# Performance work log

Measured on AMD Instinct MI355X. Metric: run time of the kernel, lower is better.

Reference implementation:

```python
import jax, jax.numpy as jnp
import numpy as np

N_NODES = 89250


def _sage_conv(x, src, dst, w_l, w_r, b):
    # mean aggregation of neighbor messages x[src] at destination nodes
    msg = x[src]                                                # [E, C]
    agg = jax.ops.segment_sum(msg, dst, num_segments=N_NODES)   # [N, C]
    cnt = jax.ops.segment_sum(jnp.ones((src.shape[0],), x.dtype), dst,
                              num_segments=N_NODES)             # [N]
    mean = agg / jnp.clip(cnt, 1.0, None)[:, None]
    # PyG SAGEConv: lin_l(aggregated) + lin_r(x) + bias
    return mean @ w_l.T + x @ w_r.T + b


def setup_inputs() -> dict:
    key = jax.random.key(0)
    ks = jax.random.split(key, 9)
    N, E, F_IN = N_NODES, 899756, 500

    def glorot(k, shape):
        fan_in = shape[1]
        return jax.random.normal(k, shape, jnp.float32) / jnp.sqrt(jnp.float32(fan_in))

    x = jax.random.normal(ks[0], (N, F_IN), jnp.float32)
    edge_index = jax.random.randint(ks[1], (2, E), 0, N, jnp.int64 if jax.config.jax_enable_x64 else jnp.int32)
    return {
        "x": x,
        "edge_index": edge_index,
        "w_l1": glorot(ks[2], (512, F_IN)),
        "w_r1": glorot(ks[3], (512, F_IN)),
        "b1": jnp.zeros((512,), jnp.float32),
        "w_l2": glorot(ks[4], (256, 512)),
        "w_r2": glorot(ks[5], (256, 512)),
        "b2": jnp.zeros((256,), jnp.float32),
        "w_l3": glorot(ks[6], (7, 256)),
        "w_r3": glorot(ks[7], (7, 256)),
        "b3": jnp.zeros((7,), jnp.float32),
    }


def reference(x, edge_index, w_l1, w_r1, b1, w_l2, w_r2, b2, w_l3, w_r3, b3):
    src, dst = edge_index[0], edge_index[1]
    # eval mode: dropout is identity
    h = jax.nn.relu(_sage_conv(x, src, dst, w_l1, w_r1, b1))
    h = jax.nn.relu(_sage_conv(h, src, dst, w_l2, w_r2, b2))
    return _sage_conv(h, src, dst, w_l3, w_r3, b3)
```

## Files before the change

kernel.cpp:

```cpp
#include <hip/hip_runtime.h>
#include <cstdint>
#include <cstddef>

#define N_NODES 89250
#define M_PAD   89344
#define F0 500
#define F1 512
#define F2 256
#define F3 7
#define KP 512

typedef __attribute__((ext_vector_type(8))) short bf16x8;
typedef __attribute__((ext_vector_type(4))) float f32x4;

static inline int cdiv_i(int a, int b) { return (a + b - 1) / b; }

__device__ __forceinline__ unsigned short f2b(float f) {
  unsigned int u = __float_as_uint(f);
  u = (u + 0x7FFFu + ((u >> 16) & 1u)) >> 16;
  return (unsigned short)u;
}
__device__ __forceinline__ float b2f(unsigned short h) {
  return __uint_as_float(((unsigned int)h) << 16);
}

__global__ void degree_kernel(const int* __restrict__ dst, int* __restrict__ cnt, int E) {
  int stride = gridDim.x * blockDim.x;
  for (int i = blockIdx.x * blockDim.x + threadIdx.x; i < E; i += stride)
    atomicAdd(&cnt[dst[i]], 1);
}

__global__ __launch_bounds__(1024) void scan_partial(const int* __restrict__ cnt,
                                                     int* __restrict__ row_ptr,
                                                     int* __restrict__ bsum, int n) {
  __shared__ int sm[1024];
  const int i = blockIdx.x * 1024 + threadIdx.x;
  const int v = (i < n) ? cnt[i] : 0;
  sm[threadIdx.x] = v;
  __syncthreads();
  for (int off = 1; off < 1024; off <<= 1) {
    int t = (threadIdx.x >= off) ? sm[threadIdx.x - off] : 0;
    __syncthreads();
    sm[threadIdx.x] += t;
    __syncthreads();
  }
  if (i < n) row_ptr[i] = sm[threadIdx.x] - v;
  if (threadIdx.x == 1023) bsum[blockIdx.x] = sm[1023];
}

__global__ __launch_bounds__(1024) void scan_bsums(int* __restrict__ bsum, int nb) {
  __shared__ int sm[1024];
  const int v = (threadIdx.x < nb) ? bsum[threadIdx.x] : 0;
  sm[threadIdx.x] = v;
  __syncthreads();
  for (int off = 1; off < 1024; off <<= 1) {
    int t = (threadIdx.x >= off) ? sm[threadIdx.x - off] : 0;
    __syncthreads();
    sm[threadIdx.x] += t;
    __syncthreads();
  }
  if (threadIdx.x < nb) bsum[threadIdx.x] = sm[threadIdx.x] - v;
}

__global__ __launch_bounds__(1024) void scan_add(int* __restrict__ row_ptr,
                                                 const int* __restrict__ bsum,
                                                 int n, int total) {
  const int i = blockIdx.x * 1024 + threadIdx.x;
  if (i < n) row_ptr[i] += bsum[i >> 10];
  if (i == 0) row_ptr[n] = total;
}

__global__ void cursor_init_kernel(const int* __restrict__ row_ptr, int* __restrict__ cursor, int n) {
  int i = blockIdx.x * blockDim.x + threadIdx.x;
  if (i < n) cursor[i] = row_ptr[i];
}

__global__ void fill_kernel(const int* __restrict__ src, const int* __restrict__ dst,
                            int* __restrict__ cursor, int* __restrict__ csr_src, int E) {
  int stride = gridDim.x * blockDim.x;
  for (int i = blockIdx.x * blockDim.x + threadIdx.x; i < E; i += stride) {
    const int p = atomicAdd(&cursor[dst[i]], 1);
    csr_src[p] = src[i];
  }
}

__global__ __launch_bounds__(256) void convert_x_kernel(const float* __restrict__ x,
                                                        unsigned short* __restrict__ xb) {
  const long long total = (long long)M_PAD * (KP / 8);
  const long long stride = (long long)gridDim.x * blockDim.x;
  for (long long idx = (long long)blockIdx.x * blockDim.x + threadIdx.x; idx < total; idx += stride) {
    const int node = (int)(idx >> 6);
    const int c8 = ((int)idx & 63) * 8;
    unsigned short r[8];
#pragma unroll
    for (int j = 0; j < 8; ++j) {
      const int c = c8 + j;
      float v = 0.0f;
      if (node < N_NODES && c < F0) v = x[(size_t)node * F0 + c];
      r[j] = f2b(v);
    }
    *reinterpret_cast<uint4*>(xb + (size_t)node * KP + c8) = *reinterpret_cast<const uint4*>(r);
  }
}

__global__ __launch_bounds__(256) void convert_w_kernel(const float* __restrict__ w,
                                                        unsigned short* __restrict__ wb,
                                                        int J, int K) {
  const int total = J * KP;
  const int stride = gridDim.x * blockDim.x;
  for (int idx = blockIdx.x * blockDim.x + threadIdx.x; idx < total; idx += stride) {
    const int j = idx >> 9;
    const int k = idx & (KP - 1);
    wb[idx] = (k < K) ? f2b(w[(size_t)j * K + k]) : (unsigned short)0;
  }
}

__global__ __launch_bounds__(256) void gather_mean_bf512(
    const unsigned short* __restrict__ xb, const int* __restrict__ row_ptr,
    const int* __restrict__ csr_src, unsigned short* __restrict__ aggb)
{
  const int node = blockIdx.x * 4 + (threadIdx.x >> 6);
  const int t = threadIdx.x & 63;
  if (node >= M_PAD) return;
  if (node >= N_NODES) {
    *reinterpret_cast<uint4*>(aggb + (size_t)node * 512 + t * 8) = make_uint4(0, 0, 0, 0);
    return;
  }
  const int beg = row_ptr[node];
  const int end = row_ptr[node + 1];
  float acc[8] = {0.f, 0.f, 0.f, 0.f, 0.f, 0.f, 0.f, 0.f};
  int j = beg;
  for (; j + 1 < end; j += 2) {
    const int s0 = csr_src[j];
    const int s1 = csr_src[j + 1];
    const uint4 v0 = *reinterpret_cast<const uint4*>(xb + (size_t)s0 * 512 + t * 8);
    const uint4 v1 = *reinterpret_cast<const uint4*>(xb + (size_t)s1 * 512 + t * 8);
    const unsigned int u0[4] = {v0.x, v0.y, v0.z, v0.w};
    const unsigned int u1[4] = {v1.x, v1.y, v1.z, v1.w};
#pragma unroll
    for (int q = 0; q < 4; ++q) {
      acc[2 * q]     += b2f((unsigned short)(u0[q] & 0xFFFF)) + b2f((unsigned short)(u1[q] & 0xFFFF));
      acc[2 * q + 1] += b2f((unsigned short)(u0[q] >> 16))    + b2f((unsigned short)(u1[q] >> 16));
    }
  }
  if (j < end) {
    const int s0 = csr_src[j];
    const uint4 v0 = *reinterpret_cast<const uint4*>(xb + (size_t)s0 * 512 + t * 8);
    const unsigned int u0[4] = {v0.x, v0.y, v0.z, v0.w};
#pragma unroll
    for (int q = 0; q < 4; ++q) {
      acc[2 * q]     += b2f((unsigned short)(u0[q] & 0xFFFF));
      acc[2 * q + 1] += b2f((unsigned short)(u0[q] >> 16));
    }
  }
  const int deg = end - beg;
  const float inv = 1.0f / (float)(deg > 1 ? deg : 1);
  unsigned short r[8];
#pragma unroll
  for (int q = 0; q < 8; ++q) r[q] = f2b(acc[q] * inv);
  *reinterpret_cast<uint4*>(aggb + (size_t)node * 512 + t * 8) = *reinterpret_cast<const uint4*>(r);
}

__global__ __launch_bounds__(256) void gemm_mfma(
    const unsigned short* __restrict__ A1, const unsigned short* __restrict__ A2,
    const unsigned short* __restrict__ B1, const unsigned short* __restrict__ B2,
    const float* __restrict__ bias, unsigned short* __restrict__ Cout,
    int J, int niter, int fuse, int relu)
{
  __shared__ __align__(16) unsigned short Alds[128 * 64];
  __shared__ __align__(16) unsigned short Blds[128 * 64];
  const int tid = threadIdx.x;
  const int lane = tid & 63;
  const int wid = tid >> 6;

  const int nwg = gridDim.x * gridDim.y;
  int wg = blockIdx.y * gridDim.x + blockIdx.x;
  const int cpx = nwg >> 3;
  wg = (wg & 7) * cpx + (wg >> 3);
  const int brow = (wg % gridDim.x) * 128;
  const int bcol = (wg / gridDim.x) * 128;

  const int wr = wid >> 1;
  const int wc = wid & 1;

  f32x4 acc[4][4];
#pragma unroll
  for (int m = 0; m < 4; ++m)
#pragma unroll
    for (int n = 0; n < 4; ++n) acc[m][n] = (f32x4){0.f, 0.f, 0.f, 0.f};

  const int srow = lane >> 3;
  const int gchunk = (lane & 7) ^ srow;
  const int fr = lane & 15;
  const int fk = lane >> 4;

  for (int it = 0; it < niter; ++it) {
    const unsigned short* __restrict__ A = (it < 8) ? A1 : A2;
    const unsigned short* __restrict__ B = (it < 8) ? B1 : B2;
    const int k0 = (it & 7) * 64;
    __syncthreads();
#pragma unroll
    for (int i = 0; i < 4; ++i) {
      const int r = i * 32 + wid * 8;
      __builtin_amdgcn_global_load_lds(
          (const __attribute__((address_space(1))) unsigned int*)(A + (size_t)(brow + r + srow) * KP + k0 + gchunk * 8),
          (__attribute__((address_space(3))) unsigned int*)(&Alds[r * 64]),
          16, 0, 0);
      __builtin_amdgcn_global_load_lds(
          (const __attribute__((address_space(1))) unsigned int*)(B + (size_t)(bcol + r + srow) * KP + k0 + gchunk * 8),
          (__attribute__((address_space(3))) unsigned int*)(&Blds[r * 64]),
          16, 0, 0);
    }
    __syncthreads();
#pragma unroll
    for (int ks = 0; ks < 2; ++ks) {
      bf16x8 a[4], b[4];
#pragma unroll
      for (int m = 0; m < 4; ++m) {
        const int row = wr * 64 + m * 16 + fr;
        a[m] = *reinterpret_cast<const bf16x8*>(&Alds[row * 64 + (((ks * 4 + fk) ^ (fr & 7)) * 8)]);
      }
#pragma unroll
      for (int n = 0; n < 4; ++n) {
        const int row = wc * 64 + n * 16 + fr;
        b[n] = *reinterpret_cast<const bf16x8*>(&Blds[row * 64 + (((ks * 4 + fk) ^ (fr & 7)) * 8)]);
      }
#pragma unroll
      for (int m = 0; m < 4; ++m)
#pragma unroll
        for (int n = 0; n < 4; ++n)
          acc[m][n] = __builtin_amdgcn_mfma_f32_16x16x32_bf16(a[m], b[n], acc[m][n], 0, 0, 0);
    }
  }

  const int crow0 = brow + wr * 64 + (lane >> 4) * 4;
  const int ccol0 = bcol + wc * 64 + (lane & 15);
#pragma unroll
  for (int n = 0; n < 4; ++n) {
    const int col = ccol0 + n * 16;
    const float bv = fuse ? bias[col] : 0.0f;
#pragma unroll
    for (int m = 0; m < 4; ++m) {
#pragma unroll
      for (int i = 0; i < 4; ++i) {
        const int row = crow0 + m * 16 + i;
        float v = acc[m][n][i] + bv;
        if (relu) v = fmaxf(v, 0.0f);
        Cout[(size_t)row * J + col] = f2b(v);
      }
    }
  }
}

__global__ __launch_bounds__(256) void combine2_kernel(
    const unsigned short* __restrict__ y, const int* __restrict__ row_ptr,
    const int* __restrict__ csr_src, const float* __restrict__ bias,
    unsigned short* __restrict__ h)
{
  const int node = blockIdx.x * 8 + (threadIdx.x >> 5);
  const int t = threadIdx.x & 31;
  if (node >= N_NODES) return;
  const int beg = row_ptr[node];
  const int end = row_ptr[node + 1];
  float acc[8] = {0.f, 0.f, 0.f, 0.f, 0.f, 0.f, 0.f, 0.f};
  int j = beg;
  for (; j + 1 < end; j += 2) {
    const int s0 = csr_src[j];
    const int s1 = csr_src[j + 1];
    const uint4 v0 = *reinterpret_cast<const uint4*>(y + (size_t)s0 * 512 + t * 8);
    const uint4 v1 = *reinterpret_cast<const uint4*>(y + (size_t)s1 * 512 + t * 8);
    const unsigned int u0[4] = {v0.x, v0.y, v0.z, v0.w};
    const unsigned int u1[4] = {v1.x, v1.y, v1.z, v1.w};
#pragma unroll
    for (int q = 0; q < 4; ++q) {
      acc[2 * q]     += b2f((unsigned short)(u0[q] & 0xFFFF)) + b2f((unsigned short)(u1[q] & 0xFFFF));
      acc[2 * q + 1] += b2f((unsigned short)(u0[q] >> 16))    + b2f((unsigned short)(u1[q] >> 16));
    }
  }
  if (j < end) {
    const int s0 = csr_src[j];
    const uint4 v0 = *reinterpret_cast<const uint4*>(y + (size_t)s0 * 512 + t * 8);
    const unsigned int u0[4] = {v0.x, v0.y, v0.z, v0.w};
#pragma unroll
    for (int q = 0; q < 4; ++q) {
      acc[2 * q]     += b2f((unsigned short)(u0[q] & 0xFFFF));
      acc[2 * q + 1] += b2f((unsigned short)(u0[q] >> 16));
    }
  }
  const int deg = end - beg;
  const float inv = 1.0f / (float)(deg > 1 ? deg : 1);
  const uint4 rv = *reinterpret_cast<const uint4*>(y + (size_t)node * 512 + 256 + t * 8);
  const unsigned int ru[4] = {rv.x, rv.y, rv.z, rv.w};
  unsigned short r[8];
#pragma unroll
  for (int q = 0; q < 4; ++q) {
    const float y0 = b2f((unsigned short)(ru[q] & 0xFFFF));
    const float y1 = b2f((unsigned short)(ru[q] >> 16));
    const float c0 = acc[2 * q] * inv + y0 + bias[t * 8 + 2 * q];
    const float c1 = acc[2 * q + 1] * inv + y1 + bias[t * 8 + 2 * q + 1];
    r[2 * q]     = f2b(fmaxf(c0, 0.0f));
    r[2 * q + 1] = f2b(fmaxf(c1, 0.0f));
  }
  *reinterpret_cast<uint4*>(h + (size_t)node * 256 + t * 8) = *reinterpret_cast<const uint4*>(r);
}

__global__ __launch_bounds__(256) void gemm3_node(
    const unsigned short* __restrict__ h2, const float* __restrict__ wl,
    const float* __restrict__ wr, unsigned short* __restrict__ y3, int N)
{
  const int node = (blockIdx.x * 256 + threadIdx.x) >> 6;
  const int lane = threadIdx.x & 63;
  if (node >= N) return;
  const uint2 hu = *reinterpret_cast<const uint2*>(h2 + (size_t)node * F2 + lane * 4);
  const float h0 = b2f((unsigned short)(hu.x & 0xFFFF)), h1 = b2f((unsigned short)(hu.x >> 16));
  const float h2v = b2f((unsigned short)(hu.y & 0xFFFF)), h3 = b2f((unsigned short)(hu.y >> 16));
#pragma unroll
  for (int j = 0; j < F3; ++j) {
    const float4 l4 = *reinterpret_cast<const float4*>(wl + j * F2 + lane * 4);
    const float4 r4 = *reinterpret_cast<const float4*>(wr + j * F2 + lane * 4);
    float tl = h0 * l4.x + h1 * l4.y + h2v * l4.z + h3 * l4.w;
    float tr = h0 * r4.x + h1 * r4.y + h2v * r4.z + h3 * r4.w;
#pragma unroll
    for (int m = 1; m < 64; m <<= 1) {
      tl += __shfl_xor(tl, m, 64);
      tr += __shfl_xor(tr, m, 64);
    }
    if (lane == 0) {
      y3[(size_t)node * 16 + j]     = f2b(tl);
      y3[(size_t)node * 16 + 8 + j] = f2b(tr);
    }
  }
}

__global__ __launch_bounds__(256) void combine3_kernel(
    const unsigned short* __restrict__ y3, const int* __restrict__ row_ptr,
    const int* __restrict__ csr_src, const float* __restrict__ b3,
    float* __restrict__ out, int N)
{
  const int node = blockIdx.x * 256 + threadIdx.x;
  if (node >= N) return;
  const int beg = row_ptr[node];
  const int end = row_ptr[node + 1];
  float acc[8] = {0.f, 0.f, 0.f, 0.f, 0.f, 0.f, 0.f, 0.f};
  for (int j = beg; j < end; ++j) {
    const int s = csr_src[j];
    const uint4 v = *reinterpret_cast<const uint4*>(y3 + (size_t)s * 16);
    const unsigned int u[4] = {v.x, v.y, v.z, v.w};
#pragma unroll
    for (int q = 0; q < 4; ++q) {
      acc[2 * q]     += b2f((unsigned short)(u[q] & 0xFFFF));
      acc[2 * q + 1] += b2f((unsigned short)(u[q] >> 16));
    }
  }
  const int deg = end - beg;
  const float inv = 1.0f / (float)(deg > 1 ? deg : 1);
  const uint4 rv = *reinterpret_cast<const uint4*>(y3 + (size_t)node * 16 + 8);
  const unsigned int ru[4] = {rv.x, rv.y, rv.z, rv.w};
  float yr[8];
#pragma unroll
  for (int q = 0; q < 4; ++q) {
    yr[2 * q]     = b2f((unsigned short)(ru[q] & 0xFFFF));
    yr[2 * q + 1] = b2f((unsigned short)(ru[q] >> 16));
  }
#pragma unroll
  for (int q = 0; q < F3; ++q)
    out[(size_t)node * F3 + q] = acc[q] * inv + yr[q] + b3[q];
}

extern "C" void kernel_launch(void* const* d_in, const int* in_sizes, int n_in,
                              void* d_out, int out_size, void* d_ws, size_t ws_size,
                              hipStream_t stream) {
  const float* x    = (const float*)d_in[0];
  const int*   ei   = (const int*)d_in[1];
  const float* w_l1 = (const float*)d_in[2];
  const float* w_r1 = (const float*)d_in[3];
  const float* b1   = (const float*)d_in[4];
  const float* w_l2 = (const float*)d_in[5];
  const float* w_r2 = (const float*)d_in[6];
  const float* b2   = (const float*)d_in[7];
  const float* w_l3 = (const float*)d_in[8];
  const float* w_r3 = (const float*)d_in[9];
  const float* b3   = (const float*)d_in[10];
  float* out = (float*)d_out;

  const int E = in_sizes[1] / 2;
  const int* src = ei;
  const int* dst = ei + E;

  char* p = (char*)d_ws;
  int* row_ptr = (int*)p;           p += (size_t)(N_NODES + 1) * 4;
  int* cnt     = (int*)p;           p += (size_t)N_NODES * 4;
  int* bsum    = (int*)p;           p += 1024 * 4;
  int* csr_src = (int*)p;           p += (size_t)E * 4;
  p = (char*)(((uintptr_t)p + 255) & ~(uintptr_t)255);
  unsigned short* xb   = (unsigned short*)p;  p += (size_t)M_PAD * KP * 2;
  unsigned short* aggb = (unsigned short*)p;  p += (size_t)M_PAD * KP * 2;
  unsigned short* h1b  = (unsigned short*)p;  p += (size_t)M_PAD * KP * 2;
  unsigned short* wl1b = (unsigned short*)p;  p += (size_t)F1 * KP * 2;
  unsigned short* wr1b = (unsigned short*)p;  p += (size_t)F1 * KP * 2;
  unsigned short* w2b  = (unsigned short*)p;  p += (size_t)F1 * KP * 2;

  unsigned short* y2  = xb;
  unsigned short* h2b = aggb;
  unsigned short* y3  = h1b;

  const int nb = cdiv_i(N_NODES, 1024);

  hipMemsetAsync(cnt, 0, (size_t)N_NODES * sizeof(int), stream);
  degree_kernel<<<cdiv_i(E, 256), 256, 0, stream>>>(dst, cnt, E);
  scan_partial<<<nb, 1024, 0, stream>>>(cnt, row_ptr, bsum, N_NODES);
  scan_bsums<<<1, 1024, 0, stream>>>(bsum, nb);
  scan_add<<<nb, 1024, 0, stream>>>(row_ptr, bsum, N_NODES, E);
  cursor_init_kernel<<<cdiv_i(N_NODES, 256), 256, 0, stream>>>(row_ptr, cnt, N_NODES);
  fill_kernel<<<cdiv_i(E, 256), 256, 0, stream>>>(src, dst, cnt, csr_src, E);

  convert_x_kernel<<<2048, 256, 0, stream>>>(x, xb);
  convert_w_kernel<<<512, 256, 0, stream>>>(w_l1, wl1b, F1, F0);
  convert_w_kernel<<<512, 256, 0, stream>>>(w_r1, wr1b, F1, F0);
  convert_w_kernel<<<256, 256, 0, stream>>>(w_l2, w2b, F2, F1);
  convert_w_kernel<<<256, 256, 0, stream>>>(w_r2, w2b + (size_t)F2 * KP, F2, F1);

  gather_mean_bf512<<<cdiv_i(M_PAD, 4), 256, 0, stream>>>(xb, row_ptr, csr_src, aggb);
  {
    dim3 g(M_PAD / 128, F1 / 128);
    gemm_mfma<<<g, 256, 0, stream>>>(aggb, xb, wl1b, wr1b, b1, h1b, F1, 16, 1, 1);
  }

  {
    dim3 g(M_PAD / 128, 512 / 128);
    gemm_mfma<<<g, 256, 0, stream>>>(h1b, h1b, w2b, w2b, (const float*)nullptr, y2, 512, 8, 0, 0);
  }
  combine2_kernel<<<cdiv_i(N_NODES, 8), 256, 0, stream>>>(y2, row_ptr, csr_src, b2, h2b);

  gemm3_node<<<cdiv_i(N_NODES * 64, 256), 256, 0, stream>>>(h2b, w_l3, w_r3, y3, N_NODES);
  combine3_kernel<<<cdiv_i(N_NODES, 256), 256, 0, stream>>>(y3, row_ptr, csr_src, b3, out, N_NODES);
}
```

Before: 707.3 us.

## Fuse cursor init into scan, unroll gathers by four, remap GEMM tiles

Folds the cursor initialisation into scan_add, which removes one kernel launch. Unrolls the neighbour-gather loops in gather_mean and combine2 from two to four edges, so more independent row loads are in flight. Switches the aggregate stores to nontemporal and changes the GEMM workgroup-to-tile mapping so that consecutive workgroups share row blocks. The four-way unroll changes the floating-point summation order slightly and raises register use.

Result: faster. 686.4 us (-3.0%).

```diff
diff --git a/kernel.cpp b/kernel.cpp
--- a/kernel.cpp
+++ b/kernel.cpp
@@ -12,6 +12,7 @@
 
 typedef __attribute__((ext_vector_type(8))) short bf16x8;
 typedef __attribute__((ext_vector_type(4))) float f32x4;
+typedef __attribute__((ext_vector_type(4))) unsigned int uintx4;
 
 static inline int cdiv_i(int a, int b) { return (a + b - 1) / b; }
 
@@ -64,15 +65,15 @@
 
 __global__ __launch_bounds__(1024) void scan_add(int* __restrict__ row_ptr,
                                                  const int* __restrict__ bsum,
+                                                 int* __restrict__ cursor,
                                                  int n, int total) {
   const int i = blockIdx.x * 1024 + threadIdx.x;
-  if (i < n) row_ptr[i] += bsum[i >> 10];
+  if (i < n) {
+    const int v = row_ptr[i] + bsum[i >> 10];
+    row_ptr[i] = v;
+    cursor[i] = v;
+  }
   if (i == 0) row_ptr[n] = total;
-}
-
-__global__ void cursor_init_kernel(const int* __restrict__ row_ptr, int* __restrict__ cursor, int n) {
-  int i = blockIdx.x * blockDim.x + threadIdx.x;
-  if (i < n) cursor[i] = row_ptr[i];
 }
 
 __global__ void fill_kernel(const int* __restrict__ src, const int* __restrict__ dst,
@@ -123,27 +124,36 @@
   const int t = threadIdx.x & 63;
   if (node >= M_PAD) return;
   if (node >= N_NODES) {
-    *reinterpret_cast<uint4*>(aggb + (size_t)node * 512 + t * 8) = make_uint4(0, 0, 0, 0);
+    uintx4 z = (uintx4){0u, 0u, 0u, 0u};
+    __builtin_nontemporal_store(z, (uintx4*)(aggb + (size_t)node * 512 + t * 8));
     return;
   }
   const int beg = row_ptr[node];
   const int end = row_ptr[node + 1];
   float acc[8] = {0.f, 0.f, 0.f, 0.f, 0.f, 0.f, 0.f, 0.f};
   int j = beg;
-  for (; j + 1 < end; j += 2) {
+  for (; j + 3 < end; j += 4) {
     const int s0 = csr_src[j];
     const int s1 = csr_src[j + 1];
+    const int s2 = csr_src[j + 2];
+    const int s3 = csr_src[j + 3];
     const uint4 v0 = *reinterpret_cast<const uint4*>(xb + (size_t)s0 * 512 + t * 8);
     const uint4 v1 = *reinterpret_cast<const uint4*>(xb + (size_t)s1 * 512 + t * 8);
+    const uint4 v2 = *reinterpret_cast<const uint4*>(xb + (size_t)s2 * 512 + t * 8);
+    const uint4 v3 = *reinterpret_cast<const uint4*>(xb + (size_t)s3 * 512 + t * 8);
     const unsigned int u0[4] = {v0.x, v0.y, v0.z, v0.w};
     const unsigned int u1[4] = {v1.x, v1.y, v1.z, v1.w};
+    const unsigned int u2[4] = {v2.x, v2.y, v2.z, v2.w};
+    const unsigned int u3[4] = {v3.x, v3.y, v3.z, v3.w};
 #pragma unroll
     for (int q = 0; q < 4; ++q) {
-      acc[2 * q]     += b2f((unsigned short)(u0[q] & 0xFFFF)) + b2f((unsigned short)(u1[q] & 0xFFFF));
-      acc[2 * q + 1] += b2f((unsigned short)(u0[q] >> 16))    + b2f((unsigned short)(u1[q] >> 16));
-    }
-  }
-  if (j < end) {
+      acc[2 * q]     += (b2f((unsigned short)(u0[q] & 0xFFFF)) + b2f((unsigned short)(u1[q] & 0xFFFF)))
+                      + (b2f((unsigned short)(u2[q] & 0xFFFF)) + b2f((unsigned short)(u3[q] & 0xFFFF)));
+      acc[2 * q + 1] += (b2f((unsigned short)(u0[q] >> 16)) + b2f((unsigned short)(u1[q] >> 16)))
+                      + (b2f((unsigned short)(u2[q] >> 16)) + b2f((unsigned short)(u3[q] >> 16)));
+    }
+  }
+  for (; j < end; ++j) {
     const int s0 = csr_src[j];
     const uint4 v0 = *reinterpret_cast<const uint4*>(xb + (size_t)s0 * 512 + t * 8);
     const unsigned int u0[4] = {v0.x, v0.y, v0.z, v0.w};
@@ -158,7 +168,8 @@
   unsigned short r[8];
 #pragma unroll
   for (int q = 0; q < 8; ++q) r[q] = f2b(acc[q] * inv);
-  *reinterpret_cast<uint4*>(aggb + (size_t)node * 512 + t * 8) = *reinterpret_cast<const uint4*>(r);
+  __builtin_nontemporal_store(*reinterpret_cast<const uintx4*>(r),
+                              (uintx4*)(aggb + (size_t)node * 512 + t * 8));
 }
 
 __global__ __launch_bounds__(256) void gemm_mfma(
@@ -177,8 +188,8 @@
   int wg = blockIdx.y * gridDim.x + blockIdx.x;
   const int cpx = nwg >> 3;
   wg = (wg & 7) * cpx + (wg >> 3);
-  const int brow = (wg % gridDim.x) * 128;
-  const int bcol = (wg / gridDim.x) * 128;
+  const int brow = (wg / gridDim.y) * 128;
+  const int bcol = (wg % gridDim.y) * 128;
 
   const int wr = wid >> 1;
   const int wc = wid & 1;
@@ -264,20 +275,28 @@
   const int end = row_ptr[node + 1];
   float acc[8] = {0.f, 0.f, 0.f, 0.f, 0.f, 0.f, 0.f, 0.f};
   int j = beg;
-  for (; j + 1 < end; j += 2) {
+  for (; j + 3 < end; j += 4) {
     const int s0 = csr_src[j];
     const int s1 = csr_src[j + 1];
+    const int s2 = csr_src[j + 2];
+    const int s3 = csr_src[j + 3];
     const uint4 v0 = *reinterpret_cast<const uint4*>(y + (size_t)s0 * 512 + t * 8);
     const uint4 v1 = *reinterpret_cast<const uint4*>(y + (size_t)s1 * 512 + t * 8);
+    const uint4 v2 = *reinterpret_cast<const uint4*>(y + (size_t)s2 * 512 + t * 8);
+    const uint4 v3 = *reinterpret_cast<const uint4*>(y + (size_t)s3 * 512 + t * 8);
     const unsigned int u0[4] = {v0.x, v0.y, v0.z, v0.w};
     const unsigned int u1[4] = {v1.x, v1.y, v1.z, v1.w};
+    const unsigned int u2[4] = {v2.x, v2.y, v2.z, v2.w};
+    const unsigned int u3[4] = {v3.x, v3.y, v3.z, v3.w};
 #pragma unroll
     for (int q = 0; q < 4; ++q) {
-      acc[2 * q]     += b2f((unsigned short)(u0[q] & 0xFFFF)) + b2f((unsigned short)(u1[q] & 0xFFFF));
-      acc[2 * q + 1] += b2f((unsigned short)(u0[q] >> 16))    + b2f((unsigned short)(u1[q] >> 16));
-    }
-  }
-  if (j < end) {
+      acc[2 * q]     += (b2f((unsigned short)(u0[q] & 0xFFFF)) + b2f((unsigned short)(u1[q] & 0xFFFF)))
+                      + (b2f((unsigned short)(u2[q] & 0xFFFF)) + b2f((unsigned short)(u3[q] & 0xFFFF)));
+      acc[2 * q + 1] += (b2f((unsigned short)(u0[q] >> 16)) + b2f((unsigned short)(u1[q] >> 16)))
+                      + (b2f((unsigned short)(u2[q] >> 16)) + b2f((unsigned short)(u3[q] >> 16)));
+    }
+  }
+  for (; j < end; ++j) {
     const int s0 = csr_src[j];
     const uint4 v0 = *reinterpret_cast<const uint4*>(y + (size_t)s0 * 512 + t * 8);
     const unsigned int u0[4] = {v0.x, v0.y, v0.z, v0.w};
@@ -410,8 +429,7 @@
   degree_kernel<<<cdiv_i(E, 256), 256, 0, stream>>>(dst, cnt, E);
   scan_partial<<<nb, 1024, 0, stream>>>(cnt, row_ptr, bsum, N_NODES);
   scan_bsums<<<1, 1024, 0, stream>>>(bsum, nb);
-  scan_add<<<nb, 1024, 0, stream>>>(row_ptr, bsum, N_NODES, E);
-  cursor_init_kernel<<<cdiv_i(N_NODES, 256), 256, 0, stream>>>(row_ptr, cnt, N_NODES);
+  scan_add<<<nb, 1024, 0, stream>>>(row_ptr, bsum, cnt, N_NODES, E);
   fill_kernel<<<cdiv_i(E, 256), 256, 0, stream>>>(src, dst, cnt, csr_src, E);
 
   convert_x_kernel<<<2048, 256, 0, stream>>>(x, xb);
```

## Unroll gathers by eight, use MFMA for layer 3, merge setup kernels

Applied to the files above, without the earlier changes.

Several changes at once. Cursor init is fused into scan_add, the four weight-convert launches become one kernel that also pre-converts layer-3 weights, and the gather loops in layer 1 and layer 2 issue eight neighbor loads at a time with masking to raise memory-level parallelism. Layer-3 projection now uses a 16x16x32 bf16 MFMA instead of shuffle reductions, combine3 spreads each node's edges across a wave, and the GEMM workgroup-to-tile mapping is swapped. The masked loads still fetch data for edges past the end of each neighbor list, and the wave-per-node combine3 adds shuffle reductions.

Result: faster. 634.0 us (-10.4%).

```diff
diff --git a/kernel.cpp b/kernel.cpp
--- a/kernel.cpp
+++ b/kernel.cpp
@@ -64,15 +64,15 @@
 
 __global__ __launch_bounds__(1024) void scan_add(int* __restrict__ row_ptr,
                                                  const int* __restrict__ bsum,
+                                                 int* __restrict__ cursor,
                                                  int n, int total) {
   const int i = blockIdx.x * 1024 + threadIdx.x;
-  if (i < n) row_ptr[i] += bsum[i >> 10];
+  if (i < n) {
+    const int v = row_ptr[i] + bsum[i >> 10];
+    row_ptr[i] = v;
+    cursor[i] = v;
+  }
   if (i == 0) row_ptr[n] = total;
-}
-
-__global__ void cursor_init_kernel(const int* __restrict__ row_ptr, int* __restrict__ cursor, int n) {
-  int i = blockIdx.x * blockDim.x + threadIdx.x;
-  if (i < n) cursor[i] = row_ptr[i];
 }
 
 __global__ void fill_kernel(const int* __restrict__ src, const int* __restrict__ dst,
@@ -103,15 +103,36 @@
   }
 }
 
-__global__ __launch_bounds__(256) void convert_w_kernel(const float* __restrict__ w,
-                                                        unsigned short* __restrict__ wb,
-                                                        int J, int K) {
-  const int total = J * KP;
-  const int stride = gridDim.x * blockDim.x;
-  for (int idx = blockIdx.x * blockDim.x + threadIdx.x; idx < total; idx += stride) {
-    const int j = idx >> 9;
-    const int k = idx & (KP - 1);
-    wb[idx] = (k < K) ? f2b(w[(size_t)j * K + k]) : (unsigned short)0;
+__global__ __launch_bounds__(256) void convert_w_all(
+    const float* __restrict__ wl1, const float* __restrict__ wr1,
+    const float* __restrict__ wl2, const float* __restrict__ wr2,
+    const float* __restrict__ wl3, const float* __restrict__ wr3,
+    unsigned short* __restrict__ wl1b, unsigned short* __restrict__ wr1b,
+    unsigned short* __restrict__ w2b, unsigned short* __restrict__ w3b)
+{
+  int idx = blockIdx.x * 256 + threadIdx.x;
+  const int S1 = F1 * KP;
+  if (idx < S1) {
+    const int j = idx >> 9, k = idx & 511;
+    const bool in = (k < F0);
+    wl1b[idx] = in ? f2b(wl1[(size_t)j * F0 + k]) : (unsigned short)0;
+    wr1b[idx] = in ? f2b(wr1[(size_t)j * F0 + k]) : (unsigned short)0;
+    return;
+  }
+  idx -= S1;
+  const int S2 = F2 * KP;
+  if (idx < S2) {
+    w2b[idx] = f2b(wl2[idx]);
+    w2b[S2 + idx] = f2b(wr2[idx]);
+    return;
+  }
+  idx -= S2;
+  if (idx < 16 * 256) {
+    const int j = idx >> 8, k = idx & 255;
+    float v = 0.0f;
+    if (j < 7) v = wl3[(size_t)j * F2 + k];
+    else if (j >= 8 && j < 15) v = wr3[(size_t)(j - 8) * F2 + k];
+    w3b[idx] = f2b(v);
   }
 }
 
@@ -129,28 +150,23 @@
   const int beg = row_ptr[node];
   const int end = row_ptr[node + 1];
   float acc[8] = {0.f, 0.f, 0.f, 0.f, 0.f, 0.f, 0.f, 0.f};
-  int j = beg;
-  for (; j + 1 < end; j += 2) {
-    const int s0 = csr_src[j];
-    const int s1 = csr_src[j + 1];
-    const uint4 v0 = *reinterpret_cast<const uint4*>(xb + (size_t)s0 * 512 + t * 8);
-    const uint4 v1 = *reinterpret_cast<const uint4*>(xb + (size_t)s1 * 512 + t * 8);
-    const unsigned int u0[4] = {v0.x, v0.y, v0.z, v0.w};
-    const unsigned int u1[4] = {v1.x, v1.y, v1.z, v1.w};
-#pragma unroll
-    for (int q = 0; q < 4; ++q) {
-      acc[2 * q]     += b2f((unsigned short)(u0[q] & 0xFFFF)) + b2f((unsigned short)(u1[q] & 0xFFFF));
-      acc[2 * q + 1] += b2f((unsigned short)(u0[q] >> 16))    + b2f((unsigned short)(u1[q] >> 16));
-    }
-  }
-  if (j < end) {
-    const int s0 = csr_src[j];
-    const uint4 v0 = *reinterpret_cast<const uint4*>(xb + (size_t)s0 * 512 + t * 8);
-    const unsigned int u0[4] = {v0.x, v0.y, v0.z, v0.w};
-#pragma unroll
-    for (int q = 0; q < 4; ++q) {
-      acc[2 * q]     += b2f((unsigned short)(u0[q] & 0xFFFF));
-      acc[2 * q + 1] += b2f((unsigned short)(u0[q] >> 16));
+  for (int j = beg; j < end; j += 8) {
+    uint4 v[8];
+    float m[8];
+#pragma unroll
+    for (int u = 0; u < 8; ++u) {
+      const int e = min(j + u, end - 1);
+      m[u] = (j + u < end) ? 1.0f : 0.0f;
+      v[u] = *reinterpret_cast<const uint4*>(xb + (size_t)csr_src[e] * 512 + t * 8);
+    }
+#pragma unroll
+    for (int u = 0; u < 8; ++u) {
+      const unsigned int w[4] = {v[u].x, v[u].y, v[u].z, v[u].w};
+#pragma unroll
+      for (int q = 0; q < 4; ++q) {
+        acc[2 * q]     = fmaf(m[u], b2f((unsigned short)(w[q] & 0xFFFF)), acc[2 * q]);
+        acc[2 * q + 1] = fmaf(m[u], b2f((unsigned short)(w[q] >> 16)),    acc[2 * q + 1]);
+      }
     }
   }
   const int deg = end - beg;
@@ -177,8 +193,8 @@
   int wg = blockIdx.y * gridDim.x + blockIdx.x;
   const int cpx = nwg >> 3;
   wg = (wg & 7) * cpx + (wg >> 3);
-  const int brow = (wg % gridDim.x) * 128;
-  const int bcol = (wg / gridDim.x) * 128;
+  const int brow = (wg / gridDim.y) * 128;
+  const int bcol = (wg % gridDim.y) * 128;
 
   const int wr = wid >> 1;
   const int wc = wid & 1;
@@ -263,28 +279,23 @@
   const int beg = row_ptr[node];
   const int end = row_ptr[node + 1];
   float acc[8] = {0.f, 0.f, 0.f, 0.f, 0.f, 0.f, 0.f, 0.f};
-  int j = beg;
-  for (; j + 1 < end; j += 2) {
-    const int s0 = csr_src[j];
-    const int s1 = csr_src[j + 1];
-    const uint4 v0 = *reinterpret_cast<const uint4*>(y + (size_t)s0 * 512 + t * 8);
-    const uint4 v1 = *reinterpret_cast<const uint4*>(y + (size_t)s1 * 512 + t * 8);
-    const unsigned int u0[4] = {v0.x, v0.y, v0.z, v0.w};
-    const unsigned int u1[4] = {v1.x, v1.y, v1.z, v1.w};
-#pragma unroll
-    for (int q = 0; q < 4; ++q) {
-      acc[2 * q]     += b2f((unsigned short)(u0[q] & 0xFFFF)) + b2f((unsigned short)(u1[q] & 0xFFFF));
-      acc[2 * q + 1] += b2f((unsigned short)(u0[q] >> 16))    + b2f((unsigned short)(u1[q] >> 16));
-    }
-  }
-  if (j < end) {
-    const int s0 = csr_src[j];
-    const uint4 v0 = *reinterpret_cast<const uint4*>(y + (size_t)s0 * 512 + t * 8);
-    const unsigned int u0[4] = {v0.x, v0.y, v0.z, v0.w};
-#pragma unroll
-    for (int q = 0; q < 4; ++q) {
-      acc[2 * q]     += b2f((unsigned short)(u0[q] & 0xFFFF));
-      acc[2 * q + 1] += b2f((unsigned short)(u0[q] >> 16));
+  for (int j = beg; j < end; j += 8) {
+    uint4 v[8];
+    float m[8];
+#pragma unroll
+    for (int u = 0; u < 8; ++u) {
+      const int e = min(j + u, end - 1);
+      m[u] = (j + u < end) ? 1.0f : 0.0f;
+      v[u] = *reinterpret_cast<const uint4*>(y + (size_t)csr_src[e] * 512 + t * 8);
+    }
+#pragma unroll
+    for (int u = 0; u < 8; ++u) {
+      const unsigned int w[4] = {v[u].x, v[u].y, v[u].z, v[u].w};
+#pragma unroll
+      for (int q = 0; q < 4; ++q) {
+        acc[2 * q]     = fmaf(m[u], b2f((unsigned short)(w[q] & 0xFFFF)), acc[2 * q]);
+        acc[2 * q + 1] = fmaf(m[u], b2f((unsigned short)(w[q] >> 16)),    acc[2 * q + 1]);
+      }
     }
   }
   const int deg = end - beg;
@@ -304,32 +315,27 @@
   *reinterpret_cast<uint4*>(h + (size_t)node * 256 + t * 8) = *reinterpret_cast<const uint4*>(r);
 }
 
-__global__ __launch_bounds__(256) void gemm3_node(
-    const unsigned short* __restrict__ h2, const float* __restrict__ wl,
-    const float* __restrict__ wr, unsigned short* __restrict__ y3, int N)
-{
-  const int node = (blockIdx.x * 256 + threadIdx.x) >> 6;
-  const int lane = threadIdx.x & 63;
-  if (node >= N) return;
-  const uint2 hu = *reinterpret_cast<const uint2*>(h2 + (size_t)node * F2 + lane * 4);
-  const float h0 = b2f((unsigned short)(hu.x & 0xFFFF)), h1 = b2f((unsigned short)(hu.x >> 16));
-  const float h2v = b2f((unsigned short)(hu.y & 0xFFFF)), h3 = b2f((unsigned short)(hu.y >> 16));
-#pragma unroll
-  for (int j = 0; j < F3; ++j) {
-    const float4 l4 = *reinterpret_cast<const float4*>(wl + j * F2 + lane * 4);
-    const float4 r4 = *reinterpret_cast<const float4*>(wr + j * F2 + lane * 4);
-    float tl = h0 * l4.x + h1 * l4.y + h2v * l4.z + h3 * l4.w;
-    float tr = h0 * r4.x + h1 * r4.y + h2v * r4.z + h3 * r4.w;
-#pragma unroll
-    for (int m = 1; m < 64; m <<= 1) {
-      tl += __shfl_xor(tl, m, 64);
-      tr += __shfl_xor(tr, m, 64);
-    }
-    if (lane == 0) {
-      y3[(size_t)node * 16 + j]     = f2b(tl);
-      y3[(size_t)node * 16 + 8 + j] = f2b(tr);
-    }
-  }
+__global__ __launch_bounds__(256) void gemm3_mfma(
+    const unsigned short* __restrict__ h2b, const unsigned short* __restrict__ w3b,
+    unsigned short* __restrict__ y3)
+{
+  const int wave = threadIdx.x >> 6, lane = threadIdx.x & 63;
+  const int rowbase = blockIdx.x * 64 + wave * 16;
+  const int fr = lane & 15, fk = lane >> 4;
+  bf16x8 b[8];
+#pragma unroll
+  for (int ks = 0; ks < 8; ++ks)
+    b[ks] = *reinterpret_cast<const bf16x8*>(w3b + fr * 256 + ks * 32 + fk * 8);
+  f32x4 acc = (f32x4){0.f, 0.f, 0.f, 0.f};
+#pragma unroll
+  for (int ks = 0; ks < 8; ++ks) {
+    const bf16x8 a = *reinterpret_cast<const bf16x8*>(h2b + (size_t)(rowbase + fr) * 256 + ks * 32 + fk * 8);
+    acc = __builtin_amdgcn_mfma_f32_16x16x32_bf16(a, b[ks], acc, 0, 0, 0);
+  }
+  const int r0 = rowbase + fk * 4;
+#pragma unroll
+  for (int i = 0; i < 4; ++i)
+    y3[(size_t)(r0 + i) * 16 + fr] = f2b(acc[i]);
 }
 
 __global__ __launch_bounds__(256) void combine3_kernel(
@@ -337,34 +343,38 @@
     const int* __restrict__ csr_src, const float* __restrict__ b3,
     float* __restrict__ out, int N)
 {
-  const int node = blockIdx.x * 256 + threadIdx.x;
+  const int node = blockIdx.x * 4 + (threadIdx.x >> 6);
+  const int lane = threadIdx.x & 63;
   if (node >= N) return;
   const int beg = row_ptr[node];
   const int end = row_ptr[node + 1];
-  float acc[8] = {0.f, 0.f, 0.f, 0.f, 0.f, 0.f, 0.f, 0.f};
-  for (int j = beg; j < end; ++j) {
+  float acc[7] = {0.f, 0.f, 0.f, 0.f, 0.f, 0.f, 0.f};
+  for (int j = beg + lane; j < end; j += 64) {
     const int s = csr_src[j];
     const uint4 v = *reinterpret_cast<const uint4*>(y3 + (size_t)s * 16);
     const unsigned int u[4] = {v.x, v.y, v.z, v.w};
 #pragma unroll
-    for (int q = 0; q < 4; ++q) {
-      acc[2 * q]     += b2f((unsigned short)(u[q] & 0xFFFF));
-      acc[2 * q + 1] += b2f((unsigned short)(u[q] >> 16));
-    }
-  }
-  const int deg = end - beg;
-  const float inv = 1.0f / (float)(deg > 1 ? deg : 1);
-  const uint4 rv = *reinterpret_cast<const uint4*>(y3 + (size_t)node * 16 + 8);
-  const unsigned int ru[4] = {rv.x, rv.y, rv.z, rv.w};
-  float yr[8];
-#pragma unroll
-  for (int q = 0; q < 4; ++q) {
-    yr[2 * q]     = b2f((unsigned short)(ru[q] & 0xFFFF));
-    yr[2 * q + 1] = b2f((unsigned short)(ru[q] >> 16));
-  }
-#pragma unroll
-  for (int q = 0; q < F3; ++q)
-    out[(size_t)node * F3 + q] = acc[q] * inv + yr[q] + b3[q];
+    for (int q = 0; q < 7; ++q) {
+      const unsigned short hw = (unsigned short)((u[q >> 1] >> ((q & 1) * 16)) & 0xFFFF);
+      acc[q] += b2f(hw);
+    }
+  }
+#pragma unroll
+  for (int q = 0; q < 7; ++q)
+#pragma unroll
+    for (int m = 1; m < 64; m <<= 1)
+      acc[q] += __shfl_xor(acc[q], m, 64);
+  if (lane == 0) {
+    const int deg = end - beg;
+    const float inv = 1.0f / (float)(deg > 1 ? deg : 1);
+    const uint4 rv = *reinterpret_cast<const uint4*>(y3 + (size_t)node * 16 + 8);
+    const unsigned int ru[4] = {rv.x, rv.y, rv.z, rv.w};
+#pragma unroll
+    for (int q = 0; q < 7; ++q) {
+      const float self = b2f((unsigned short)((ru[q >> 1] >> ((q & 1) * 16)) & 0xFFFF));
+      out[(size_t)node * F3 + q] = acc[q] * inv + self + b3[q];
+    }
+  }
 }
 
 extern "C" void kernel_launch(void* const* d_in, const int* in_sizes, int n_in,
@@ -399,6 +409,7 @@
   unsigned short* wl1b = (unsigned short*)p;  p += (size_t)F1 * KP * 2;
   unsigned short* wr1b = (unsigned short*)p;  p += (size_t)F1 * KP * 2;
   unsigned short* w2b  = (unsigned short*)p;  p += (size_t)F1 * KP * 2;
+  unsigned short* w3b  = (unsigned short*)p;  p += (size_t)16 * F2 * 2;
 
   unsigned short* y2  = xb;
   unsigned short* h2b = aggb;
@@ -410,15 +421,15 @@
   degree_kernel<<<cdiv_i(E, 256), 256, 0, stream>>>(dst, cnt, E);
   scan_partial<<<nb, 1024, 0, stream>>>(cnt, row_ptr, bsum, N_NODES);
   scan_bsums<<<1, 1024, 0, stream>>>(bsum, nb);
-  scan_add<<<nb, 1024, 0, stream>>>(row_ptr, bsum, N_NODES, E);
-  cursor_init_kernel<<<cdiv_i(N_NODES, 256), 256, 0, stream>>>(row_ptr, cnt, N_NODES);
+  scan_add<<<nb, 1024, 0, stream>>>(row_ptr, bsum, cnt, N_NODES, E);
   fill_kernel<<<cdiv_i(E, 256), 256, 0, stream>>>(src, dst, cnt, csr_src, E);
 
   convert_x_kernel<<<2048, 256, 0, stream>>>(x, xb);
-  convert_w_kernel<<<512, 256, 0, stream>>>(w_l1, wl1b, F1, F0);
-  convert_w_kernel<<<512, 256, 0, stream>>>(w_r1, wr1b, F1, F0);
-  convert_w_kernel<<<256, 256, 0, stream>>>(w_l2, w2b, F2, F1);
-  convert_w_kernel<<<256, 256, 0, stream>>>(w_r2, w2b + (size_t)F2 * KP, F2, F1);
+  {
+    const int total = F1 * KP + F2 * KP + 16 * F2;
+    convert_w_all<<<cdiv_i(total, 256), 256, 0, stream>>>(
+        w_l1, w_r1, w_l2, w_r2, w_l3, w_r3, wl1b, wr1b, w2b, w3b);
+  }
 
   gather_mean_bf512<<<cdiv_i(M_PAD, 4), 256, 0, stream>>>(xb, row_ptr, csr_src, aggb);
   {
@@ -432,6 +443,6 @@
   }
   combine2_kernel<<<cdiv_i(N_NODES, 8), 256, 0, stream>>>(y2, row_ptr, csr_src, b2, h2b);
 
-  gemm3_node<<<cdiv_i(N_NODES * 64, 256), 256, 0, stream>>>(h2b, w_l3, w_r3, y3, N_NODES);
-  combine3_kernel<<<cdiv_i(N_NODES, 256), 256, 0, stream>>>(y3, row_ptr, csr_src, b3, out, N_NODES);
-}
+  gemm3_mfma<<<M_PAD / 64, 256, 0, stream>>>(h2b, w3b, y3);
+  combine3_kernel<<<cdiv_i(N_NODES, 4), 256, 0, stream>>>(y3, row_ptr, csr_src, b3, out, N_NODES);
+}
```
